# Optimization experiments

Measured on AMD Instinct MI355X. Metric: run time of the kernel, lower is better.

## Reference

```python
import jax, jax.numpy as jnp
import numpy as np

NUM_EXPERTS = 8
TOP_K = 2

def setup_inputs() -> dict:
    key = jax.random.key(0)
    k1, k2, k3, k4 = jax.random.split(key, 4)
    B, L, D, F, E = 2, 2048, 1024, 2048, NUM_EXPERTS
    layer_input = jax.random.normal(k1, (B, L, D), dtype=jnp.float32)
    router_w = jax.random.normal(k2, (E, D), dtype=jnp.float32) * 0.02
    # input_linear.weight.transpose(2,1) in torch -> [E, D, 2F] layout here
    w1 = jax.random.normal(k3, (E, D, 2 * F), dtype=jnp.float32) * 0.02
    # output_linear.weight.transpose(2,1) -> [E, F, D]
    w2 = jax.random.normal(k4, (E, F, D), dtype=jnp.float32) * 0.02
    return {"layer_input": layer_input, "router_w": router_w, "w1": w1, "w2": w2}


def reference(layer_input, router_w, w1, w2):
    B, L, D = layer_input.shape
    E = router_w.shape[0]
    x = layer_input.reshape(-1, D)                              # [N, D]
    router_logits = x @ router_w.T                              # [N, E]
    probs = jax.nn.softmax(router_logits.astype(jnp.float32), axis=-1)
    routing_weights, selected = jax.lax.top_k(probs, TOP_K)     # [N, K]
    routing_weights = routing_weights / routing_weights.sum(-1, keepdims=True)
    routing_weights = routing_weights.astype(x.dtype)

    out = jnp.zeros_like(x)
    # Fixed small loop over experts; same math as sorted grouped-GEMM + scatter-combine.
    for e in range(E):
        gate_e = jnp.sum(jnp.where(selected == e, routing_weights, 0.0), axis=-1)  # [N]
        gh = x @ w1[e]                                          # [N, 2F]
        g, h = jnp.split(gh, 2, axis=-1)
        y = (jax.nn.silu(g) * h) @ w2[e]                        # [N, D]
        out = out + gate_e[:, None] * y
    return out.reshape(B, L, D)
```

## Files before the change

kernel.cpp:

```cpp
#include <hip/hip_runtime.h>
#include <stdint.h>

typedef unsigned short u16;
typedef __attribute__((ext_vector_type(8))) short short8;
typedef __attribute__((ext_vector_type(4))) float floatx4;

#define NTOK 4096
#define DDIM 1024
#define FDIM 2048
#define NEXP 8

__device__ __forceinline__ u16 f2bf(float f) {
    union { float f; uint32_t u; } v; v.f = f;
    uint32_t r = v.u + 0x7fff + ((v.u >> 16) & 1);
    return (u16)(r >> 16);
}
__device__ __forceinline__ uint32_t pk2(float a, float b) {
    return (uint32_t)f2bf(a) | ((uint32_t)f2bf(b) << 16);
}
__device__ __forceinline__ void gl_lds16(const u16* g, u16* l) {
    __builtin_amdgcn_global_load_lds(
        (const __attribute__((address_space(1))) uint32_t*)g,
        (__attribute__((address_space(3))) uint32_t*)l, 16, 0, 0);
}

__global__ __launch_bounds__(256)
void router_kernel(const float* __restrict__ x, const float* __restrict__ rw,
                   int* __restrict__ topk_e, float* __restrict__ topk_w,
                   u16* __restrict__ xb) {
    const int lane = threadIdx.x & 63;
    const int wv = threadIdx.x >> 6;
    const int tok = blockIdx.x * 4 + wv;
    const float* xr = x + (size_t)tok * DDIM;
    u16* xo = xb + (size_t)tok * DDIM;
    float acc[8];
#pragma unroll
    for (int e = 0; e < 8; ++e) acc[e] = 0.f;
#pragma unroll
    for (int it = 0; it < 4; ++it) {
        int d0 = (it * 64 + lane) * 4;
        float4 xv = *(const float4*)(xr + d0);
        uint2 o = { pk2(xv.x, xv.y), pk2(xv.z, xv.w) };
        *(uint2*)(xo + d0) = o;
#pragma unroll
        for (int e = 0; e < 8; ++e) {
            float4 wv4 = *(const float4*)(rw + (size_t)e * DDIM + d0);
            acc[e] += xv.x * wv4.x + xv.y * wv4.y + xv.z * wv4.z + xv.w * wv4.w;
        }
    }
#pragma unroll
    for (int s = 32; s > 0; s >>= 1)
#pragma unroll
        for (int e = 0; e < 8; ++e) acc[e] += __shfl_down(acc[e], s);
    if (lane == 0) {
        int e0 = 0;
#pragma unroll
        for (int e = 1; e < 8; ++e) if (acc[e] > acc[e0]) e0 = e;
        int e1 = (e0 == 0) ? 1 : 0;
#pragma unroll
        for (int e = 0; e < 8; ++e) if (e != e0 && acc[e] > acc[e1]) e1 = e;
        float w0 = 1.f / (1.f + __expf(acc[e1] - acc[e0]));
        topk_e[tok * 2 + 0] = e0;
        topk_e[tok * 2 + 1] = e1;
        topk_w[tok * 2 + 0] = w0;
        topk_w[tok * 2 + 1] = 1.f - w0;
    }
}

__global__ __launch_bounds__(256)
void prefix_kernel(const int* __restrict__ topk_e, int* __restrict__ counts,
                   int* __restrict__ offs, int* __restrict__ cursors) {
    __shared__ int h[NEXP];
    const int t = threadIdx.x;
    if (t < NEXP) h[t] = 0;
    __syncthreads();
    int c[NEXP];
#pragma unroll
    for (int j = 0; j < NEXP; ++j) c[j] = 0;
    const int4* te4 = (const int4*)topk_e;
#pragma unroll
    for (int it = 0; it < 8; ++it) {
        int4 v = te4[it * 256 + t];
#pragma unroll
        for (int j = 0; j < NEXP; ++j)
            c[j] += (v.x == j) + (v.y == j) + (v.z == j) + (v.w == j);
    }
#pragma unroll
    for (int j = 0; j < NEXP; ++j)
        if (c[j]) atomicAdd(&h[j], c[j]);
    __syncthreads();
    if (t == 0) {
        int s = 0;
        for (int e = 0; e < NEXP; ++e) {
            counts[e] = h[e];
            offs[e] = s;
            s += h[e];
        }
        offs[NEXP] = s;
    }
    if (t < NEXP) cursors[t] = 0;
}

__global__ __launch_bounds__(256)
void build_rows(const int* __restrict__ topk_e, const int* __restrict__ offs,
                int* __restrict__ cursors, int* __restrict__ row_tok,
                float* __restrict__ gate_row, const float* __restrict__ topk_w) {
    __shared__ int lcnt[NEXP];
    __shared__ int lbase[NEXP];
    const int t = threadIdx.x;
    if (t < NEXP) lcnt[t] = 0;
    __syncthreads();
    const int tok = blockIdx.x * 256 + t;
    const int e0 = topk_e[tok * 2 + 0];
    const int e1 = topk_e[tok * 2 + 1];
    const int s0 = atomicAdd(&lcnt[e0], 1);
    const int s1 = atomicAdd(&lcnt[e1], 1);
    __syncthreads();
    if (t < NEXP) lbase[t] = lcnt[t] ? atomicAdd(&cursors[t], lcnt[t]) : 0;
    __syncthreads();
    int r0 = offs[e0] + lbase[e0] + s0;
    row_tok[r0] = tok;
    gate_row[r0] = topk_w[tok * 2 + 0];
    int r1 = offs[e1] + lbase[e1] + s1;
    row_tok[r1] = tok;
    gate_row[r1] = topk_w[tok * 2 + 1];
}

__global__ __launch_bounds__(256)
void transpose_f32_bf16(const float* __restrict__ src, u16* __restrict__ dst,
                        int R, int C) {
    __shared__ float tile[64][65];
    size_t eo = (size_t)blockIdx.z * R * C;
    const float* S = src + eo;
    u16* D = dst + eo;
    int r0 = blockIdx.y * 64, c0 = blockIdx.x * 64;
    int t = threadIdx.x;
    int rr = t >> 4;
    int cc = (t & 15) * 4;
#pragma unroll
    for (int it = 0; it < 4; ++it) {
        int r = rr + it * 16;
        float4 v = *(const float4*)(S + (size_t)(r0 + r) * C + (c0 + cc));
        tile[cc + 0][r] = v.x; tile[cc + 1][r] = v.y;
        tile[cc + 2][r] = v.z; tile[cc + 3][r] = v.w;
    }
    __syncthreads();
#pragma unroll
    for (int it = 0; it < 2; ++it) {
        int u = it * 256 + t;
        int c = u >> 3;
        int rv = (u & 7) * 8;
        uint4 o;
        o.x = pk2(tile[c][rv + 0], tile[c][rv + 1]);
        o.y = pk2(tile[c][rv + 2], tile[c][rv + 3]);
        o.z = pk2(tile[c][rv + 4], tile[c][rv + 5]);
        o.w = pk2(tile[c][rv + 6], tile[c][rv + 7]);
        *(uint4*)(D + (size_t)(c0 + c) * R + (r0 + rv)) = o;
    }
}

__global__ __launch_bounds__(256, 2)
void gemm1_fast(const u16* __restrict__ xb, const u16* __restrict__ w1b,
                u16* __restrict__ act, const int* __restrict__ row_tok,
                const int* __restrict__ counts, const int* __restrict__ offs) {
    const int bid = blockIdx.x;
    const int e = bid & 7;
    const int cnt = counts[e];
    const int nmb = (cnt + 127) >> 7;
    const int j = bid >> 3;
    if (j >= nmb * 32) return;
    const int m0 = (j % nmb) * 128;
    const int n0 = (j / nmb) * 64;
    const int off = offs[e];

    __shared__ __align__(16) u16 As[2 * 128 * 32];
    __shared__ __align__(16) u16 Bs[2 * 128 * 32];

    const int t = threadIdx.x;
    const int lane = t & 63;
    const int wv = t >> 6;
    const int quad = lane >> 4;
    const int rr = lane & 15;
    const int wm = (wv & 1) * 64;
    const int wn = (wv >> 1) * 32;

    const int scol = (((lane & 3) ^ ((lane >> 3) & 3)) * 8);
    const int xq = (quad ^ ((rr >> 1) & 3)) * 8;
    const u16* arA[2];
    const u16* arB[2];
#pragma unroll
    for (int i = 0; i < 2; ++i) {
        int m = wv * 32 + i * 16 + ((lane >> 2) & 15);
        int r = m0 + m; if (r >= cnt) r = cnt - 1;
        arA[i] = xb + (size_t)row_tok[off + r] * DDIM + scol;
        size_t brow = (m < 64) ? ((size_t)e * 4096 + n0 + m)
                               : ((size_t)e * 4096 + 2048 + n0 + (m - 64));
        arB[i] = w1b + brow * DDIM + scol;
    }
    u16* dstA[2][2];
    u16* dstB[2][2];
#pragma unroll
    for (int s = 0; s < 2; ++s)
#pragma unroll
        for (int i = 0; i < 2; ++i) {
            dstA[s][i] = &As[(s * 128 + wv * 32 + i * 16) * 32];
            dstB[s][i] = &Bs[(s * 128 + wv * 32 + i * 16) * 32];
        }

    floatx4 accg[4][2] = {};
    floatx4 acch[4][2] = {};

    for (int k0 = 0; k0 < DDIM; k0 += 64) {
        __syncthreads();
#pragma unroll
        for (int s = 0; s < 2; ++s)
#pragma unroll
            for (int i = 0; i < 2; ++i) {
                gl_lds16(arA[i] + k0 + s * 32, dstA[s][i]);
                gl_lds16(arB[i] + k0 + s * 32, dstB[s][i]);
            }
        __syncthreads();

#pragma unroll
        for (int s = 0; s < 2; ++s) {
            short8 af[4], bg[2], bh[2];
#pragma unroll
            for (int mt = 0; mt < 4; ++mt)
                af[mt] = *(const short8*)&As[(s * 128 + wm + mt * 16 + rr) * 32 + xq];
#pragma unroll
            for (int nt = 0; nt < 2; ++nt) {
                bg[nt] = *(const short8*)&Bs[(s * 128 + wn + nt * 16 + rr) * 32 + xq];
                bh[nt] = *(const short8*)&Bs[(s * 128 + 64 + wn + nt * 16 + rr) * 32 + xq];
            }
#pragma unroll
            for (int mt = 0; mt < 4; ++mt)
#pragma unroll
                for (int nt = 0; nt < 2; ++nt) {
                    accg[mt][nt] = __builtin_amdgcn_mfma_f32_16x16x32_bf16(af[mt], bg[nt], accg[mt][nt], 0, 0, 0);
                    acch[mt][nt] = __builtin_amdgcn_mfma_f32_16x16x32_bf16(af[mt], bh[nt], acch[mt][nt], 0, 0, 0);
                }
        }
    }
#pragma unroll
    for (int mt = 0; mt < 4; ++mt)
#pragma unroll
        for (int nt = 0; nt < 2; ++nt)
#pragma unroll
            for (int rg = 0; rg < 4; ++rg) {
                int gm = m0 + wm + mt * 16 + quad * 4 + rg;
                if (gm < cnt) {
                    float g = accg[mt][nt][rg];
                    float h = acch[mt][nt][rg];
                    float s = g / (1.f + __expf(-g));
                    act[(size_t)(off + gm) * FDIM + (n0 + wn + nt * 16 + rr)] = f2bf(s * h);
                }
            }
}

__global__ __launch_bounds__(256, 2)
void gemm2_fast(const u16* __restrict__ act, const u16* __restrict__ w2b,
                float* __restrict__ out, const int* __restrict__ row_tok,
                const float* __restrict__ gate_row, const int* __restrict__ counts,
                const int* __restrict__ offs) {
    const int bid = blockIdx.x;
    const int e = bid & 7;
    const int cnt = counts[e];
    const int nmb = (cnt + 127) >> 7;
    const int j = bid >> 3;
    if (j >= nmb * 8) return;
    const int m0 = (j % nmb) * 128;
    const int n0 = (j / nmb) * 128;
    const int off = offs[e];

    __shared__ __align__(16) u16 As[2 * 128 * 32];
    __shared__ __align__(16) u16 Bs[2 * 128 * 32];

    const int t = threadIdx.x;
    const int lane = t & 63;
    const int wv = t >> 6;
    const int quad = lane >> 4;
    const int rr = lane & 15;
    const int wm = (wv & 1) * 64;
    const int wn = (wv >> 1) * 64;

    const int scol = (((lane & 3) ^ ((lane >> 3) & 3)) * 8);
    const int xq = (quad ^ ((rr >> 1) & 3)) * 8;
    const u16* arA[2];
    const u16* arB[2];
#pragma unroll
    for (int i = 0; i < 2; ++i) {
        int m = wv * 32 + i * 16 + ((lane >> 2) & 15);
        int r = m0 + m; if (r >= cnt) r = cnt - 1;
        arA[i] = act + (size_t)(off + r) * FDIM + scol;
        arB[i] = w2b + ((size_t)e * 1024 + n0 + m) * FDIM + scol;
    }
    u16* dstA[2][2];
    u16* dstB[2][2];
#pragma unroll
    for (int s = 0; s < 2; ++s)
#pragma unroll
        for (int i = 0; i < 2; ++i) {
            dstA[s][i] = &As[(s * 128 + wv * 32 + i * 16) * 32];
            dstB[s][i] = &Bs[(s * 128 + wv * 32 + i * 16) * 32];
        }

    floatx4 acc[4][4] = {};

    for (int k0 = 0; k0 < FDIM; k0 += 64) {
        __syncthreads();
#pragma unroll
        for (int s = 0; s < 2; ++s)
#pragma unroll
            for (int i = 0; i < 2; ++i) {
                gl_lds16(arA[i] + k0 + s * 32, dstA[s][i]);
                gl_lds16(arB[i] + k0 + s * 32, dstB[s][i]);
            }
        __syncthreads();

#pragma unroll
        for (int s = 0; s < 2; ++s) {
            short8 af[4], bf[4];
#pragma unroll
            for (int mt = 0; mt < 4; ++mt)
                af[mt] = *(const short8*)&As[(s * 128 + wm + mt * 16 + rr) * 32 + xq];
#pragma unroll
            for (int nt = 0; nt < 4; ++nt)
                bf[nt] = *(const short8*)&Bs[(s * 128 + wn + nt * 16 + rr) * 32 + xq];
#pragma unroll
            for (int mt = 0; mt < 4; ++mt)
#pragma unroll
                for (int nt = 0; nt < 4; ++nt)
                    acc[mt][nt] = __builtin_amdgcn_mfma_f32_16x16x32_bf16(af[mt], bf[nt], acc[mt][nt], 0, 0, 0);
        }
    }
#pragma unroll
    for (int mt = 0; mt < 4; ++mt)
#pragma unroll
        for (int rg = 0; rg < 4; ++rg) {
            int gm = m0 + wm + mt * 16 + quad * 4 + rg;
            if (gm < cnt) {
                int gr = off + gm;
                float gate = gate_row[gr];
                float* orow = out + (size_t)row_tok[gr] * DDIM + n0 + wn;
#pragma unroll
                for (int nt = 0; nt < 4; ++nt)
                    atomicAdd(&orow[nt * 16 + rr], gate * acc[mt][nt][rg]);
            }
        }
}

extern "C" void kernel_launch(void* const* d_in, const int* in_sizes, int n_in,
                              void* d_out, int out_size, void* d_ws, size_t ws_size,
                              hipStream_t stream) {
    const float* x  = (const float*)d_in[0];
    const float* rw = (const float*)d_in[1];
    const float* w1 = (const float*)d_in[2];
    const float* w2 = (const float*)d_in[3];
    float* out = (float*)d_out;

    char* ws = (char*)d_ws;
    const size_t MB = 1ull << 20;
    int*   counts   = (int*)(ws);
    int*   cursors  = (int*)(ws + 64);
    int*   offs     = (int*)(ws + 128);
    int*   topk_e   = (int*)(ws + 2048);
    float* topk_w   = (float*)(ws + 2048 + 32768);
    int*   row_tok  = (int*)(ws + 2048 + 65536);
    float* gate_row = (float*)(ws + 2048 + 98304);
    u16*   act      = (u16*)(ws + 1 * MB);
    u16*   xb       = (u16*)(ws + 33 * MB);
    u16*   w1b      = (u16*)(ws + 41 * MB);
    u16*   w2b      = (u16*)(ws + 41 * MB);

    hipMemsetAsync(out, 0, (size_t)out_size * 4, stream);
    router_kernel<<<dim3(NTOK / 4), 256, 0, stream>>>(x, rw, topk_e, topk_w, xb);
    prefix_kernel<<<1, 256, 0, stream>>>(topk_e, counts, offs, cursors);
    build_rows<<<dim3(NTOK / 256), 256, 0, stream>>>(topk_e, offs, cursors, row_tok, gate_row, topk_w);
    transpose_f32_bf16<<<dim3(4096 / 64, 1024 / 64, NEXP), 256, 0, stream>>>(w1, w1b, 1024, 4096);
    gemm1_fast<<<dim3(8192), 256, 0, stream>>>(xb, w1b, act, row_tok, counts, offs);
    transpose_f32_bf16<<<dim3(1024 / 64, 2048 / 64, NEXP), 256, 0, stream>>>(w2, w2b, 2048, 1024);
    gemm2_fast<<<dim3(2048), 256, 0, stream>>>(act, w2b, out, row_tok, gate_row, counts, offs);
    (void)in_sizes; (void)n_in; (void)ws_size;
}
```

Baseline: 440.6 us.

## Replace atomic scatter-add in second GEMM with per-row store plus combine kernel

The second expert GEMM now writes its fp32 results to a per-routed-row scratch buffer with plain stores instead of gate-weighted atomicAdds into the output. A new combine kernel gathers each token's two expert rows, applies the routing weights and writes the output. This also drops the output memset. It removes atomic contention and makes the output deterministic, at the cost of a 32 MB scratch write and read plus one more launch.

```diff
diff --git a/kernel.cpp b/kernel.cpp
--- a/kernel.cpp
+++ b/kernel.cpp
@@ -104,7 +104,7 @@
 __global__ __launch_bounds__(256)
 void build_rows(const int* __restrict__ topk_e, const int* __restrict__ offs,
                 int* __restrict__ cursors, int* __restrict__ row_tok,
-                float* __restrict__ gate_row, const float* __restrict__ topk_w) {
+                int* __restrict__ tok_row) {
     __shared__ int lcnt[NEXP];
     __shared__ int lbase[NEXP];
     const int t = threadIdx.x;
@@ -120,10 +120,10 @@
     __syncthreads();
     int r0 = offs[e0] + lbase[e0] + s0;
     row_tok[r0] = tok;
-    gate_row[r0] = topk_w[tok * 2 + 0];
+    tok_row[tok * 2 + 0] = r0;
     int r1 = offs[e1] + lbase[e1] + s1;
     row_tok[r1] = tok;
-    gate_row[r1] = topk_w[tok * 2 + 1];
+    tok_row[tok * 2 + 1] = r1;
 }
 
 __global__ __launch_bounds__(256)
@@ -259,8 +259,7 @@
 
 __global__ __launch_bounds__(256, 2)
 void gemm2_fast(const u16* __restrict__ act, const u16* __restrict__ w2b,
-                float* __restrict__ out, const int* __restrict__ row_tok,
-                const float* __restrict__ gate_row, const int* __restrict__ counts,
+                float* __restrict__ y, const int* __restrict__ counts,
                 const int* __restrict__ offs) {
     const int bid = blockIdx.x;
     const int e = bid & 7;
@@ -339,14 +338,28 @@
         for (int rg = 0; rg < 4; ++rg) {
             int gm = m0 + wm + mt * 16 + quad * 4 + rg;
             if (gm < cnt) {
-                int gr = off + gm;
-                float gate = gate_row[gr];
-                float* orow = out + (size_t)row_tok[gr] * DDIM + n0 + wn;
+                float* yrow = y + (size_t)(off + gm) * DDIM + n0 + wn;
 #pragma unroll
                 for (int nt = 0; nt < 4; ++nt)
-                    atomicAdd(&orow[nt * 16 + rr], gate * acc[mt][nt][rg]);
-            }
-        }
+                    yrow[nt * 16 + rr] = acc[mt][nt][rg];
+            }
+        }
+}
+
+__global__ __launch_bounds__(256)
+void combine_kernel(const float* __restrict__ y, const int* __restrict__ tok_row,
+                    const float* __restrict__ topk_w, float* __restrict__ out) {
+    const int tok = blockIdx.x;
+    const int t = threadIdx.x;
+    const int r0 = tok_row[tok * 2 + 0];
+    const int r1 = tok_row[tok * 2 + 1];
+    const float w0 = topk_w[tok * 2 + 0];
+    const float w1 = topk_w[tok * 2 + 1];
+    float4 a = *(const float4*)(y + (size_t)r0 * DDIM + t * 4);
+    float4 b = *(const float4*)(y + (size_t)r1 * DDIM + t * 4);
+    float4 o = { w0 * a.x + w1 * b.x, w0 * a.y + w1 * b.y,
+                 w0 * a.z + w1 * b.z, w0 * a.w + w1 * b.w };
+    *(float4*)(out + (size_t)tok * DDIM + t * 4) = o;
 }
 
 extern "C" void kernel_launch(void* const* d_in, const int* in_sizes, int n_in,
@@ -366,19 +379,20 @@
     int*   topk_e   = (int*)(ws + 2048);
     float* topk_w   = (float*)(ws + 2048 + 32768);
     int*   row_tok  = (int*)(ws + 2048 + 65536);
-    float* gate_row = (float*)(ws + 2048 + 98304);
+    int*   tok_row  = (int*)(ws + 2048 + 98304);
     u16*   act      = (u16*)(ws + 1 * MB);
     u16*   xb       = (u16*)(ws + 33 * MB);
     u16*   w1b      = (u16*)(ws + 41 * MB);
     u16*   w2b      = (u16*)(ws + 41 * MB);
-
-    hipMemsetAsync(out, 0, (size_t)out_size * 4, stream);
+    float* yb       = (float*)(ws + 73 * MB);
+
     router_kernel<<<dim3(NTOK / 4), 256, 0, stream>>>(x, rw, topk_e, topk_w, xb);
     prefix_kernel<<<1, 256, 0, stream>>>(topk_e, counts, offs, cursors);
-    build_rows<<<dim3(NTOK / 256), 256, 0, stream>>>(topk_e, offs, cursors, row_tok, gate_row, topk_w);
+    build_rows<<<dim3(NTOK / 256), 256, 0, stream>>>(topk_e, offs, cursors, row_tok, tok_row);
     transpose_f32_bf16<<<dim3(4096 / 64, 1024 / 64, NEXP), 256, 0, stream>>>(w1, w1b, 1024, 4096);
     gemm1_fast<<<dim3(8192), 256, 0, stream>>>(xb, w1b, act, row_tok, counts, offs);
     transpose_f32_bf16<<<dim3(1024 / 64, 2048 / 64, NEXP), 256, 0, stream>>>(w2, w2b, 2048, 1024);
-    gemm2_fast<<<dim3(2048), 256, 0, stream>>>(act, w2b, out, row_tok, gate_row, counts, offs);
+    gemm2_fast<<<dim3(2048), 256, 0, stream>>>(act, w2b, yb, counts, offs);
+    combine_kernel<<<dim3(NTOK), 256, 0, stream>>>(yb, tok_row, topk_w, out);
     (void)in_sizes; (void)n_in; (void)ws_size;
 }
```

Result: faster. 431.4 us (-2.1%).
